# Optimization experiments

Hardware: AMD Instinct MI355X
Metric: run time of the kernel (lower is better)

## Reference

```python
import jax, jax.numpy as jnp
import numpy as np

D_MODEL = 1024
NUM_HEADS = 16
D_K = D_MODEL // NUM_HEADS
D_FF = 4096
EPS = 1e-5


def _layernorm(x, gamma, beta):
    mu = jnp.mean(x, axis=-1, keepdims=True)
    var = jnp.mean(jnp.square(x - mu), axis=-1, keepdims=True)
    return (x - mu) * jax.lax.rsqrt(var + EPS) * gamma + beta


def setup_inputs() -> dict:
    key = jax.random.key(0)
    ks = jax.random.split(key, 16)
    B, S = 4, 2048
    s_in = 1.0 / np.sqrt(D_MODEL)
    s_ff = 1.0 / np.sqrt(D_FF)
    inp = {
        "x": jax.random.normal(ks[0], (B, S, D_MODEL), jnp.float32),
        "src_mask": jnp.ones((B, 1, 1, S), jnp.int32),
        "w_q": jax.random.normal(ks[1], (D_MODEL, D_MODEL), jnp.float32) * s_in,
        "b_q": jnp.zeros((D_MODEL,), jnp.float32),
        "w_k": jax.random.normal(ks[2], (D_MODEL, D_MODEL), jnp.float32) * s_in,
        "b_k": jnp.zeros((D_MODEL,), jnp.float32),
        "w_v": jax.random.normal(ks[3], (D_MODEL, D_MODEL), jnp.float32) * s_in,
        "b_v": jnp.zeros((D_MODEL,), jnp.float32),
        "w_o": jax.random.normal(ks[4], (D_MODEL, D_MODEL), jnp.float32) * s_in,
        "b_o": jnp.zeros((D_MODEL,), jnp.float32),
        "w1": jax.random.normal(ks[5], (D_MODEL, D_FF), jnp.float32) * s_in,
        "b1": jnp.zeros((D_FF,), jnp.float32),
        "w2": jax.random.normal(ks[6], (D_FF, D_MODEL), jnp.float32) * s_ff,
        "b2": jnp.zeros((D_MODEL,), jnp.float32),
        "g1": jnp.ones((D_MODEL,), jnp.float32),
        "be1": jnp.zeros((D_MODEL,), jnp.float32),
        "g2": jnp.ones((D_MODEL,), jnp.float32),
        "be2": jnp.zeros((D_MODEL,), jnp.float32),
    }
    return inp


def reference(x, src_mask, w_q, b_q, w_k, b_k, w_v, b_v, w_o, b_o,
              w1, b1, w2, b2, g1, be1, g2, be2):
    B, S, _ = x.shape

    def split_heads(t):  # [B,S,D] -> [B,H,S,dk]
        return t.reshape(B, S, NUM_HEADS, D_K).transpose(0, 2, 1, 3)

    q = split_heads(x @ w_q + b_q)
    k = split_heads(x @ w_k + b_k)
    v = split_heads(x @ w_v + b_v)

    scores = jnp.einsum("bhqd,bhkd->bhqk", q, k) / np.sqrt(D_K)
    scores = jnp.where(src_mask == 0, -jnp.inf, scores)
    attn = jax.nn.softmax(scores, axis=-1)
    ctx = jnp.einsum("bhqk,bhkd->bhqd", attn, v)
    merged = ctx.transpose(0, 2, 1, 3).reshape(B, S, D_MODEL)
    attn_out = merged @ w_o + b_o

    h = _layernorm(x + attn_out, g1, be1)
    ff = jax.nn.relu(h @ w1 + b1) @ w2 + b2
    return _layernorm(h + ff, g2, be2)
```

## Files before the change

### kernel.cpp

```cpp
#include <hip/hip_runtime.h>

typedef unsigned short u16;
typedef __attribute__((ext_vector_type(4))) unsigned short u16x4;
typedef __attribute__((ext_vector_type(8))) short bf16x8;
typedef __attribute__((ext_vector_type(4))) float f32x4;

__device__ inline float bf2f(u16 u) {
  union { unsigned int i; float f; } v; v.i = ((unsigned int)u) << 16; return v.f;
}
__device__ inline u16 f2bf(float f) {
  union { float f; unsigned int i; } v; v.f = f;
  unsigned int r = v.i + 0x7fffu + ((v.i >> 16) & 1u);
  return (u16)(r >> 16);
}

typedef const __attribute__((address_space(1))) unsigned int* gas_t;
typedef __attribute__((address_space(3))) unsigned int* las_t;
__device__ inline void gload_lds16(const u16* g, u16* l) {
  __builtin_amdgcn_global_load_lds((gas_t)(unsigned long long)(const void*)g,
                                   (las_t)(unsigned int)(unsigned long long)(void*)l,
                                   16, 0, 0);
}

__global__ __launch_bounds__(256) void cvt_bf16(const float* __restrict__ src,
                                                u16* __restrict__ dst, int n) {
  int i = (blockIdx.x * 256 + threadIdx.x) * 4;
  if (i >= n) return;
  float4 v = *(const float4*)(src + i);
  u16x4 o;
  o.x = f2bf(v.x); o.y = f2bf(v.y); o.z = f2bf(v.z); o.w = f2bf(v.w);
  *(u16x4*)(dst + i) = o;
}

__global__ __launch_bounds__(256) void concat3(const float* __restrict__ a,
                                               const float* __restrict__ b,
                                               const float* __restrict__ c,
                                               float* __restrict__ o, int n) {
  int i = blockIdx.x * 256 + threadIdx.x;
  if (i >= n) return;
  o[i] = a[i]; o[n + i] = b[i]; o[2 * n + i] = c[i];
}

__global__ __launch_bounds__(256) void transpose_f32_bf16(const float* __restrict__ src,
                                                          u16* __restrict__ dst,
                                                          int R, int C) {
  __shared__ u16 tile[32][33];
  int tx = threadIdx.x & 31, ty = threadIdx.x >> 5;
  int c0 = blockIdx.x * 32, r0 = blockIdx.y * 32;
  #pragma unroll
  for (int i = ty; i < 32; i += 8)
    tile[i][tx] = f2bf(src[(size_t)(r0 + i) * C + c0 + tx]);
  __syncthreads();
  #pragma unroll
  for (int i = ty; i < 32; i += 8)
    dst[(size_t)(c0 + i) * R + r0 + tx] = tile[tx][i];
}

__global__ __launch_bounds__(256) void transpose_v(const u16* __restrict__ src,
                                                   u16* __restrict__ VT,
                                                   int B, int S, int H, int RS, int CO) {
  __shared__ u16 tile[32][33];
  int tx = threadIdx.x & 31, ty = threadIdx.x >> 5;
  int s0 = blockIdx.x * 32, d0 = blockIdx.y * 32;
  int bh = blockIdx.z;
  int b = bh / H, h = bh % H;
  #pragma unroll
  for (int i = ty; i < 32; i += 8)
    tile[i][tx] = src[(size_t)(b * S + s0 + i) * RS + CO + h * 64 + d0 + tx];
  __syncthreads();
  #pragma unroll
  for (int i = ty; i < 32; i += 8)
    VT[((size_t)bh * 64 + d0 + i) * S + s0 + tx] = tile[tx][i];
}

__global__ __launch_bounds__(256) void gemm_bt(const u16* __restrict__ A,
                                               const u16* __restrict__ Bt,
                                               const float* __restrict__ bias,
                                               u16* __restrict__ C,
                                               int M, int N, int K, int relu) {
  __shared__ u16 As[128 * 32];
  __shared__ u16 Bs[128 * 32];
  const int tid = threadIdx.x;
  const int lane = tid & 63, wid = tid >> 6;
  const int lr = lane & 15, quad = lane >> 4;
  const int wm = (wid >> 1) * 64, wn = (wid & 1) * 64;
  const int m0 = blockIdx.y * 128, n0 = blockIdx.x * 128;
  const int lrow = lane >> 2;
  const int lcol = (lane & 3) * 8;

  f32x4 acc[4][4];
  const f32x4 zero = {0.f, 0.f, 0.f, 0.f};
  #pragma unroll
  for (int mt = 0; mt < 4; ++mt)
    #pragma unroll
    for (int nt = 0; nt < 4; ++nt) acc[mt][nt] = zero;

  for (int k0 = 0; k0 < K; k0 += 32) {
    #pragma unroll
    for (int it = 0; it < 2; ++it) {
      int rbase = wid * 32 + it * 16;
      gload_lds16(A + (size_t)(m0 + rbase + lrow) * K + k0 + lcol, &As[rbase * 32]);
      gload_lds16(Bt + (size_t)(n0 + rbase + lrow) * K + k0 + lcol, &Bs[rbase * 32]);
    }
    __syncthreads();
    bf16x8 af[4], bfr[4];
    #pragma unroll
    for (int mt = 0; mt < 4; ++mt)
      af[mt] = *(const bf16x8*)(&As[(wm + mt * 16 + lr) * 32 + quad * 8]);
    #pragma unroll
    for (int nt = 0; nt < 4; ++nt)
      bfr[nt] = *(const bf16x8*)(&Bs[(wn + nt * 16 + lr) * 32 + quad * 8]);
    #pragma unroll
    for (int mt = 0; mt < 4; ++mt)
      #pragma unroll
      for (int nt = 0; nt < 4; ++nt)
        acc[mt][nt] = __builtin_amdgcn_mfma_f32_16x16x32_bf16(af[mt], bfr[nt], acc[mt][nt], 0, 0, 0);
    __syncthreads();
  }

  #pragma unroll
  for (int nt = 0; nt < 4; ++nt) {
    int n = n0 + wn + nt * 16 + lr;
    float bv = bias[n];
    #pragma unroll
    for (int mt = 0; mt < 4; ++mt) {
      #pragma unroll
      for (int i = 0; i < 4; ++i) {
        int m = m0 + wm + mt * 16 + quad * 4 + i;
        float v = acc[mt][nt][i] + bv;
        if (relu) v = fmaxf(v, 0.f);
        C[(size_t)m * N + n] = f2bf(v);
      }
    }
  }
}

__global__ __launch_bounds__(256) void flash_attn(const u16* __restrict__ Qp,
                                                  const u16* __restrict__ Kp,
                                                  const u16* __restrict__ VT,
                                                  const int* __restrict__ mask,
                                                  u16* __restrict__ ctx,
                                                  int B, int S, int H, int QSTR) {
  __shared__ u16 kt_lds[64 * 72];
  __shared__ u16 vt_lds[64 * 72];
  __shared__ u16 p_lds[4 * 16 * 72];
  __shared__ float msk_lds[64];
  const int tid = threadIdx.x;
  const int lane = tid & 63, wid = tid >> 6;
  const int lr = lane & 15, quad = lane >> 4;
  const int bh = blockIdx.y;
  const int b = bh / H, h = bh % H;
  const int q0 = blockIdx.x * 64;
  const u16* vt_base = VT + (size_t)bh * 64 * S;

  bf16x8 qf[2];
  {
    int qm = q0 + wid * 16 + lr;
    const u16* qptr = Qp + (size_t)(b * S + qm) * QSTR + h * 64;
    qf[0] = *(const bf16x8*)(qptr + quad * 8);
    qf[1] = *(const bf16x8*)(qptr + 32 + quad * 8);
  }

  float m_i = -1e30f, l_i = 0.f;
  float O[4][4];
  #pragma unroll
  for (int nt = 0; nt < 4; ++nt)
    #pragma unroll
    for (int i = 0; i < 4; ++i) O[nt][i] = 0.f;

  for (int kt = 0; kt < S; kt += 64) {
    #pragma unroll
    for (int it = 0; it < 2; ++it) {
      int c = tid + it * 256;
      int r = c >> 3;
      int cc = (c & 7) * 8;
      uint4 kv = *(const uint4*)(Kp + (size_t)(b * S + kt + r) * QSTR + h * 64 + cc);
      *(uint4*)(&kt_lds[r * 72 + cc]) = kv;
      uint4 vv = *(const uint4*)(vt_base + (size_t)r * S + kt + cc);
      *(uint4*)(&vt_lds[r * 72 + cc]) = vv;
    }
    if (tid < 64) msk_lds[tid] = mask[b * S + kt + tid] ? 0.f : -1e30f;
    __syncthreads();

    float s[4][4];
    #pragma unroll
    for (int st = 0; st < 4; ++st) {
      f32x4 c = {0.f, 0.f, 0.f, 0.f};
      #pragma unroll
      for (int ch = 0; ch < 2; ++ch) {
        bf16x8 kf = *(const bf16x8*)(&kt_lds[(st * 16 + lr) * 72 + ch * 32 + quad * 8]);
        c = __builtin_amdgcn_mfma_f32_16x16x32_bf16(kf, qf[ch], c, 0, 0, 0);
      }
      float4 mv = *(const float4*)(&msk_lds[st * 16 + quad * 4]);
      s[st][0] = c[0] * 0.125f + mv.x;
      s[st][1] = c[1] * 0.125f + mv.y;
      s[st][2] = c[2] * 0.125f + mv.z;
      s[st][3] = c[3] * 0.125f + mv.w;
    }

    float tmax = s[0][0];
    #pragma unroll
    for (int st = 0; st < 4; ++st)
      #pragma unroll
      for (int i = 0; i < 4; ++i) tmax = fmaxf(tmax, s[st][i]);
    tmax = fmaxf(tmax, __shfl_xor(tmax, 16, 64));
    tmax = fmaxf(tmax, __shfl_xor(tmax, 32, 64));
    float mn = fmaxf(m_i, tmax);
    float al = __expf(m_i - mn);
    m_i = mn;
    float rs = 0.f;
    #pragma unroll
    for (int st = 0; st < 4; ++st)
      #pragma unroll
      for (int i = 0; i < 4; ++i) {
        float p = __expf(s[st][i] - mn);
        s[st][i] = p; rs += p;
      }
    rs += __shfl_xor(rs, 16, 64);
    rs += __shfl_xor(rs, 32, 64);
    l_i = l_i * al + rs;

    u16* pw = &p_lds[wid * 16 * 72];
    #pragma unroll
    for (int st = 0; st < 4; ++st) {
      u16x4 pk;
      pk.x = f2bf(s[st][0]); pk.y = f2bf(s[st][1]);
      pk.z = f2bf(s[st][2]); pk.w = f2bf(s[st][3]);
      *(u16x4*)(&pw[lr * 72 + st * 16 + quad * 4]) = pk;
    }

    #pragma unroll
    for (int nt = 0; nt < 4; ++nt) {
      f32x4 c;
      c[0] = O[nt][0] * al; c[1] = O[nt][1] * al;
      c[2] = O[nt][2] * al; c[3] = O[nt][3] * al;
      #pragma unroll
      for (int ch = 0; ch < 2; ++ch) {
        bf16x8 vf = *(const bf16x8*)(&vt_lds[(nt * 16 + lr) * 72 + ch * 32 + quad * 8]);
        bf16x8 pf = *(const bf16x8*)(&pw[lr * 72 + ch * 32 + quad * 8]);
        c = __builtin_amdgcn_mfma_f32_16x16x32_bf16(vf, pf, c, 0, 0, 0);
      }
      O[nt][0] = c[0]; O[nt][1] = c[1]; O[nt][2] = c[2]; O[nt][3] = c[3];
    }
    __syncthreads();
  }

  float linv = 1.f / fmaxf(l_i, 1e-30f);
  int q = q0 + wid * 16 + lr;
  u16* op = ctx + (size_t)(b * S + q) * (H * 64) + h * 64;
  #pragma unroll
  for (int nt = 0; nt < 4; ++nt) {
    u16x4 o;
    o.x = f2bf(O[nt][0] * linv); o.y = f2bf(O[nt][1] * linv);
    o.z = f2bf(O[nt][2] * linv); o.w = f2bf(O[nt][3] * linv);
    *(u16x4*)(op + nt * 16 + quad * 4) = o;
  }
}

__device__ inline float block_reduce_sum(float v, float* sbuf) {
  #pragma unroll
  for (int m = 1; m < 64; m <<= 1) v += __shfl_xor(v, m, 64);
  int w = threadIdx.x >> 6;
  if ((threadIdx.x & 63) == 0) sbuf[w] = v;
  __syncthreads();
  v = sbuf[0] + sbuf[1] + sbuf[2] + sbuf[3];
  __syncthreads();
  return v;
}

__global__ __launch_bounds__(256) void add_ln(const float* __restrict__ a32,
                                              const u16* __restrict__ a16,
                                              const u16* __restrict__ b,
                                              const float* __restrict__ g,
                                              const float* __restrict__ be,
                                              u16* __restrict__ out16,
                                              float* __restrict__ out32, int D) {
  __shared__ float sbuf[4];
  int row = blockIdx.x;
  size_t base = (size_t)row * D;
  int i = threadIdx.x * 4;
  float v[4];
  {
    u16x4 bv = *(const u16x4*)(b + base + i);
    if (a32) {
      float4 av = *(const float4*)(a32 + base + i);
      v[0] = av.x + bf2f(bv.x); v[1] = av.y + bf2f(bv.y);
      v[2] = av.z + bf2f(bv.z); v[3] = av.w + bf2f(bv.w);
    } else {
      u16x4 av = *(const u16x4*)(a16 + base + i);
      v[0] = bf2f(av.x) + bf2f(bv.x); v[1] = bf2f(av.y) + bf2f(bv.y);
      v[2] = bf2f(av.z) + bf2f(bv.z); v[3] = bf2f(av.w) + bf2f(bv.w);
    }
  }
  float sum = v[0] + v[1] + v[2] + v[3];
  sum = block_reduce_sum(sum, sbuf);
  float mean = sum / (float)D;
  float var = 0.f;
  #pragma unroll
  for (int j = 0; j < 4; ++j) { float d = v[j] - mean; var += d * d; }
  var = block_reduce_sum(var, sbuf);
  float rstd = rsqrtf(var / (float)D + 1e-5f);
  float4 gv = *(const float4*)(g + i);
  float4 bev = *(const float4*)(be + i);
  float o0 = (v[0] - mean) * rstd * gv.x + bev.x;
  float o1 = (v[1] - mean) * rstd * gv.y + bev.y;
  float o2 = (v[2] - mean) * rstd * gv.z + bev.z;
  float o3 = (v[3] - mean) * rstd * gv.w + bev.w;
  if (out32) {
    float4 o = {o0, o1, o2, o3};
    *(float4*)(out32 + base + i) = o;
  } else {
    u16x4 o;
    o.x = f2bf(o0); o.y = f2bf(o1); o.z = f2bf(o2); o.w = f2bf(o3);
    *(u16x4*)(out16 + base + i) = o;
  }
}

extern "C" void kernel_launch(void* const* d_in, const int* in_sizes, int n_in,
                              void* d_out, int out_size, void* d_ws, size_t ws_size,
                              hipStream_t stream) {
  (void)in_sizes; (void)n_in; (void)out_size; (void)ws_size;
  const float* x   = (const float*)d_in[0];
  const int* mask  = (const int*)d_in[1];
  const float* wq  = (const float*)d_in[2];
  const float* bq  = (const float*)d_in[3];
  const float* wk  = (const float*)d_in[4];
  const float* bk  = (const float*)d_in[5];
  const float* wv  = (const float*)d_in[6];
  const float* bv  = (const float*)d_in[7];
  const float* wo  = (const float*)d_in[8];
  const float* bo  = (const float*)d_in[9];
  const float* w1  = (const float*)d_in[10];
  const float* b1  = (const float*)d_in[11];
  const float* w2  = (const float*)d_in[12];
  const float* b2  = (const float*)d_in[13];
  const float* g1  = (const float*)d_in[14];
  const float* be1 = (const float*)d_in[15];
  const float* g2  = (const float*)d_in[16];
  const float* be2 = (const float*)d_in[17];

  const int B = 4, S = 2048, D = 1024, H = 16, DFF = 4096;
  const int D3 = 3 * D;
  const size_t TOK = (size_t)B * S;
  const size_t TD = TOK * D;

  u16* ws   = (u16*)d_ws;
  u16* QKVp = ws;
  u16* xb   = ws + 3 * TD;
  u16* VT   = xb;
  u16* CTX  = ws + 4 * TD;
  u16* ATT  = ws + 5 * TD;
  u16* Hb   = ws + 6 * TD;
  u16* QKVT = ws + 7 * TD;
  u16* WOT  = QKVT + 3 * (size_t)D * D;
  u16* W1T  = WOT + (size_t)D * D;
  u16* FF1  = ws;
  u16* FF2  = ATT;
  u16* W2T  = QKVT;
  float* biasc = (float*)CTX;

  dim3 blk(256);

  cvt_bf16<<<dim3((unsigned)(TD / (256 * 4))), blk, 0, stream>>>(x, xb, (int)TD);
  concat3<<<dim3(4), blk, 0, stream>>>(bq, bk, bv, biasc, D);

  transpose_f32_bf16<<<dim3(D / 32, D / 32), blk, 0, stream>>>(wq, QKVT, D, D);
  transpose_f32_bf16<<<dim3(D / 32, D / 32), blk, 0, stream>>>(wk, QKVT + (size_t)D * D, D, D);
  transpose_f32_bf16<<<dim3(D / 32, D / 32), blk, 0, stream>>>(wv, QKVT + 2 * (size_t)D * D, D, D);
  transpose_f32_bf16<<<dim3(D / 32, D / 32), blk, 0, stream>>>(wo, WOT, D, D);
  transpose_f32_bf16<<<dim3(DFF / 32, D / 32), blk, 0, stream>>>(w1, W1T, D, DFF);

  gemm_bt<<<dim3(D3 / 128, TOK / 128), blk, 0, stream>>>(xb, QKVT, biasc, QKVp, (int)TOK, D3, D, 0);

  transpose_v<<<dim3(S / 32, 2, B * H), blk, 0, stream>>>(QKVp, VT, B, S, H, D3, 2 * D);

  flash_attn<<<dim3(S / 64, B * H), blk, 0, stream>>>(QKVp, QKVp + D, VT, mask, CTX, B, S, H, D3);

  gemm_bt<<<dim3(D / 128, TOK / 128), blk, 0, stream>>>(CTX, WOT, bo, ATT, (int)TOK, D, D, 0);

  transpose_f32_bf16<<<dim3(D / 32, DFF / 32), blk, 0, stream>>>(w2, W2T, DFF, D);

  add_ln<<<dim3((unsigned)TOK), blk, 0, stream>>>(x, (const u16*)nullptr, ATT, g1, be1,
                                                  Hb, (float*)nullptr, D);

  gemm_bt<<<dim3(DFF / 128, TOK / 128), blk, 0, stream>>>(Hb, W1T, b1, FF1, (int)TOK, DFF, D, 1);
  gemm_bt<<<dim3(D / 128, TOK / 128), blk, 0, stream>>>(FF1, W2T, b2, FF2, (int)TOK, D, DFF, 0);

  add_ln<<<dim3((unsigned)TOK), blk, 0, stream>>>((const float*)nullptr, Hb, FF2, g2, be2,
                                                  (u16*)nullptr, (float*)d_out, D);
}
```

Before: 669.4 us.

## Process two query tiles per wave in flash attention and use exp2 softmax

Each wave in flash_attn now handles 32 query rows instead of 16, and each block handles 128 queries, so the launch grid is halved. The K and V fragments loaded from LDS are reused across both query tiles, which cuts LDS reads and global K/V traffic per query. The softmax scale now folds in log2(e) so exp2f can be used, and P is packed to bf16 with a cheaper perm-based round-half-up instead of round-to-nearest-even. In exchange each thread holds more registers, which can lower occupancy, and the rounding of P changes slightly.

```diff
diff --git a/kernel.cpp b/kernel.cpp
--- a/kernel.cpp
+++ b/kernel.cpp
@@ -12,6 +12,10 @@
   union { float f; unsigned int i; } v; v.f = f;
   unsigned int r = v.i + 0x7fffu + ((v.i >> 16) & 1u);
   return (u16)(r >> 16);
+}
+__device__ inline unsigned int pack2bf(float lo, float hi) {
+  union { float f; unsigned int i; } a, b; a.f = lo; b.f = hi;
+  return __builtin_amdgcn_perm(b.i + 0x8000u, a.i + 0x8000u, 0x07060302u);
 }
 
 typedef const __attribute__((address_space(1))) unsigned int* gas_t;
@@ -143,30 +147,36 @@
                                                   int B, int S, int H, int QSTR) {
   __shared__ u16 kt_lds[64 * 72];
   __shared__ u16 vt_lds[64 * 72];
-  __shared__ u16 p_lds[4 * 16 * 72];
+  __shared__ u16 p_lds[4 * 32 * 72];
   __shared__ float msk_lds[64];
   const int tid = threadIdx.x;
   const int lane = tid & 63, wid = tid >> 6;
   const int lr = lane & 15, quad = lane >> 4;
   const int bh = blockIdx.y;
   const int b = bh / H, h = bh % H;
-  const int q0 = blockIdx.x * 64;
+  const int q0 = blockIdx.x * 128;
   const u16* vt_base = VT + (size_t)bh * 64 * S;
-
-  bf16x8 qf[2];
-  {
-    int qm = q0 + wid * 16 + lr;
+  const float SC = 0.125f * 1.44269504089f;
+
+  bf16x8 qf[2][2];
+  #pragma unroll
+  for (int f = 0; f < 2; ++f) {
+    int qm = q0 + wid * 32 + f * 16 + lr;
     const u16* qptr = Qp + (size_t)(b * S + qm) * QSTR + h * 64;
-    qf[0] = *(const bf16x8*)(qptr + quad * 8);
-    qf[1] = *(const bf16x8*)(qptr + 32 + quad * 8);
-  }
-
-  float m_i = -1e30f, l_i = 0.f;
-  float O[4][4];
-  #pragma unroll
-  for (int nt = 0; nt < 4; ++nt)
-    #pragma unroll
-    for (int i = 0; i < 4; ++i) O[nt][i] = 0.f;
+    qf[f][0] = *(const bf16x8*)(qptr + quad * 8);
+    qf[f][1] = *(const bf16x8*)(qptr + 32 + quad * 8);
+  }
+
+  float m_i[2] = {-1e30f, -1e30f}, l_i[2] = {0.f, 0.f};
+  float O[2][4][4];
+  #pragma unroll
+  for (int f = 0; f < 2; ++f)
+    #pragma unroll
+    for (int nt = 0; nt < 4; ++nt)
+      #pragma unroll
+      for (int i = 0; i < 4; ++i) O[f][nt][i] = 0.f;
+
+  u16* pw = &p_lds[wid * 32 * 72];
 
   for (int kt = 0; kt < S; kt += 64) {
     #pragma unroll
@@ -182,78 +192,96 @@
     if (tid < 64) msk_lds[tid] = mask[b * S + kt + tid] ? 0.f : -1e30f;
     __syncthreads();
 
-    float s[4][4];
+    float s[2][4][4];
     #pragma unroll
     for (int st = 0; st < 4; ++st) {
-      f32x4 c = {0.f, 0.f, 0.f, 0.f};
-      #pragma unroll
-      for (int ch = 0; ch < 2; ++ch) {
-        bf16x8 kf = *(const bf16x8*)(&kt_lds[(st * 16 + lr) * 72 + ch * 32 + quad * 8]);
-        c = __builtin_amdgcn_mfma_f32_16x16x32_bf16(kf, qf[ch], c, 0, 0, 0);
+      bf16x8 kf0 = *(const bf16x8*)(&kt_lds[(st * 16 + lr) * 72 + quad * 8]);
+      bf16x8 kf1 = *(const bf16x8*)(&kt_lds[(st * 16 + lr) * 72 + 32 + quad * 8]);
+      float4 mv = *(const float4*)(&msk_lds[st * 16 + quad * 4]);
+      #pragma unroll
+      for (int f = 0; f < 2; ++f) {
+        f32x4 c = {0.f, 0.f, 0.f, 0.f};
+        c = __builtin_amdgcn_mfma_f32_16x16x32_bf16(kf0, qf[f][0], c, 0, 0, 0);
+        c = __builtin_amdgcn_mfma_f32_16x16x32_bf16(kf1, qf[f][1], c, 0, 0, 0);
+        s[f][st][0] = c[0] * SC + mv.x;
+        s[f][st][1] = c[1] * SC + mv.y;
+        s[f][st][2] = c[2] * SC + mv.z;
+        s[f][st][3] = c[3] * SC + mv.w;
       }
-      float4 mv = *(const float4*)(&msk_lds[st * 16 + quad * 4]);
-      s[st][0] = c[0] * 0.125f + mv.x;
-      s[st][1] = c[1] * 0.125f + mv.y;
-      s[st][2] = c[2] * 0.125f + mv.z;
-      s[st][3] = c[3] * 0.125f + mv.w;
-    }
-
-    float tmax = s[0][0];
-    #pragma unroll
-    for (int st = 0; st < 4; ++st)
-      #pragma unroll
-      for (int i = 0; i < 4; ++i) tmax = fmaxf(tmax, s[st][i]);
-    tmax = fmaxf(tmax, __shfl_xor(tmax, 16, 64));
-    tmax = fmaxf(tmax, __shfl_xor(tmax, 32, 64));
-    float mn = fmaxf(m_i, tmax);
-    float al = __expf(m_i - mn);
-    m_i = mn;
-    float rs = 0.f;
-    #pragma unroll
-    for (int st = 0; st < 4; ++st)
-      #pragma unroll
-      for (int i = 0; i < 4; ++i) {
-        float p = __expf(s[st][i] - mn);
-        s[st][i] = p; rs += p;
+    }
+
+    float al[2];
+    #pragma unroll
+    for (int f = 0; f < 2; ++f) {
+      float tmax = s[f][0][0];
+      #pragma unroll
+      for (int st = 0; st < 4; ++st)
+        #pragma unroll
+        for (int i = 0; i < 4; ++i) tmax = fmaxf(tmax, s[f][st][i]);
+      tmax = fmaxf(tmax, __shfl_xor(tmax, 16, 64));
+      tmax = fmaxf(tmax, __shfl_xor(tmax, 32, 64));
+      float mn = fmaxf(m_i[f], tmax);
+      al[f] = exp2f(m_i[f] - mn);
+      m_i[f] = mn;
+      float rs = 0.f;
+      #pragma unroll
+      for (int st = 0; st < 4; ++st)
+        #pragma unroll
+        for (int i = 0; i < 4; ++i) {
+          float p = exp2f(s[f][st][i] - mn);
+          s[f][st][i] = p; rs += p;
+        }
+      rs += __shfl_xor(rs, 16, 64);
+      rs += __shfl_xor(rs, 32, 64);
+      l_i[f] = l_i[f] * al[f] + rs;
+    }
+
+    #pragma unroll
+    for (int f = 0; f < 2; ++f) {
+      #pragma unroll
+      for (int st = 0; st < 4; ++st) {
+        uint2 pk;
+        pk.x = pack2bf(s[f][st][0], s[f][st][1]);
+        pk.y = pack2bf(s[f][st][2], s[f][st][3]);
+        *(uint2*)(&pw[(f * 16 + lr) * 72 + st * 16 + quad * 4]) = pk;
       }
-    rs += __shfl_xor(rs, 16, 64);
-    rs += __shfl_xor(rs, 32, 64);
-    l_i = l_i * al + rs;
-
-    u16* pw = &p_lds[wid * 16 * 72];
-    #pragma unroll
-    for (int st = 0; st < 4; ++st) {
-      u16x4 pk;
-      pk.x = f2bf(s[st][0]); pk.y = f2bf(s[st][1]);
-      pk.z = f2bf(s[st][2]); pk.w = f2bf(s[st][3]);
-      *(u16x4*)(&pw[lr * 72 + st * 16 + quad * 4]) = pk;
-    }
-
+    }
+
+    bf16x8 pf[2][2];
+    #pragma unroll
+    for (int f = 0; f < 2; ++f) {
+      pf[f][0] = *(const bf16x8*)(&pw[(f * 16 + lr) * 72 + quad * 8]);
+      pf[f][1] = *(const bf16x8*)(&pw[(f * 16 + lr) * 72 + 32 + quad * 8]);
+    }
     #pragma unroll
     for (int nt = 0; nt < 4; ++nt) {
-      f32x4 c;
-      c[0] = O[nt][0] * al; c[1] = O[nt][1] * al;
-      c[2] = O[nt][2] * al; c[3] = O[nt][3] * al;
-      #pragma unroll
-      for (int ch = 0; ch < 2; ++ch) {
-        bf16x8 vf = *(const bf16x8*)(&vt_lds[(nt * 16 + lr) * 72 + ch * 32 + quad * 8]);
-        bf16x8 pf = *(const bf16x8*)(&pw[lr * 72 + ch * 32 + quad * 8]);
-        c = __builtin_amdgcn_mfma_f32_16x16x32_bf16(vf, pf, c, 0, 0, 0);
+      bf16x8 vf0 = *(const bf16x8*)(&vt_lds[(nt * 16 + lr) * 72 + quad * 8]);
+      bf16x8 vf1 = *(const bf16x8*)(&vt_lds[(nt * 16 + lr) * 72 + 32 + quad * 8]);
+      #pragma unroll
+      for (int f = 0; f < 2; ++f) {
+        f32x4 c;
+        c[0] = O[f][nt][0] * al[f]; c[1] = O[f][nt][1] * al[f];
+        c[2] = O[f][nt][2] * al[f]; c[3] = O[f][nt][3] * al[f];
+        c = __builtin_amdgcn_mfma_f32_16x16x32_bf16(vf0, pf[f][0], c, 0, 0, 0);
+        c = __builtin_amdgcn_mfma_f32_16x16x32_bf16(vf1, pf[f][1], c, 0, 0, 0);
+        O[f][nt][0] = c[0]; O[f][nt][1] = c[1]; O[f][nt][2] = c[2]; O[f][nt][3] = c[3];
       }
-      O[nt][0] = c[0]; O[nt][1] = c[1]; O[nt][2] = c[2]; O[nt][3] = c[3];
     }
     __syncthreads();
   }
 
-  float linv = 1.f / fmaxf(l_i, 1e-30f);
-  int q = q0 + wid * 16 + lr;
-  u16* op = ctx + (size_t)(b * S + q) * (H * 64) + h * 64;
-  #pragma unroll
-  for (int nt = 0; nt < 4; ++nt) {
-    u16x4 o;
-    o.x = f2bf(O[nt][0] * linv); o.y = f2bf(O[nt][1] * linv);
-    o.z = f2bf(O[nt][2] * linv); o.w = f2bf(O[nt][3] * linv);
-    *(u16x4*)(op + nt * 16 + quad * 4) = o;
+  #pragma unroll
+  for (int f = 0; f < 2; ++f) {
+    float linv = 1.f / fmaxf(l_i[f], 1e-30f);
+    int q = q0 + wid * 32 + f * 16 + lr;
+    u16* op = ctx + (size_t)(b * S + q) * (H * 64) + h * 64;
+    #pragma unroll
+    for (int nt = 0; nt < 4; ++nt) {
+      u16x4 o;
+      o.x = f2bf(O[f][nt][0] * linv); o.y = f2bf(O[f][nt][1] * linv);
+      o.z = f2bf(O[f][nt][2] * linv); o.w = f2bf(O[f][nt][3] * linv);
+      *(u16x4*)(op + nt * 16 + quad * 4) = o;
+    }
   }
 }
 
@@ -374,7 +402,7 @@
 
   transpose_v<<<dim3(S / 32, 2, B * H), blk, 0, stream>>>(QKVp, VT, B, S, H, D3, 2 * D);
 
-  flash_attn<<<dim3(S / 64, B * H), blk, 0, stream>>>(QKVp, QKVp + D, VT, mask, CTX, B, S, H, D3);
+  flash_attn<<<dim3(S / 128, B * H), blk, 0, stream>>>(QKVp, QKVp + D, VT, mask, CTX, B, S, H, D3);
 
   gemm_bt<<<dim3(D / 128, TOK / 128), blk, 0, stream>>>(CTX, WOT, bo, ATT, (int)TOK, D, D, 0);
 
```

Result: slower. 722.1 us (+7.9%).
